# Kernel optimization log

Measured on AMD Instinct MI355X. Metric: run time of the kernel, lower is better.

## Reference

```python
import jax, jax.numpy as jnp
import numpy as np

B, N, H, E, D = 8, 2048, 1024, 8, 2048


def setup_inputs() -> dict:
    key = jax.random.key(0)
    k = jax.random.split(key, 5)
    x = jax.random.normal(k[0], (B, N, H), dtype=jnp.float32)
    Wr = jax.random.normal(k[1], (H, E), dtype=jnp.float32) * 0.02
    br = jnp.zeros((E,), dtype=jnp.float32)
    W1 = jax.random.normal(k[2], (E, H, D), dtype=jnp.float32) * 0.02
    b1 = jnp.zeros((E, D), dtype=jnp.float32)
    W2 = jax.random.normal(k[3], (E, D, H), dtype=jnp.float32) * 0.02
    b2 = jnp.zeros((E, H), dtype=jnp.float32)
    return {"x": x, "Wr": Wr, "br": br, "W1": W1, "b1": b1, "W2": W2, "b2": b2}


def reference(x, Wr, br, W1, b1, W2, b2):
    # x: [B,N,H]; router v1, top-1, eval mode (no expert dropout)
    Bx, Nx, Hx = x.shape
    Ex = Wr.shape[1]
    x_flat = x.reshape(Bx * Nx, Hx)                      # [T,H]
    logits = x_flat @ Wr + br                            # [T,E]
    probs = jax.nn.softmax(logits, axis=-1)              # [T,E]
    expert_idx = jnp.argmax(probs, axis=-1)              # [T]

    out_flat = jnp.zeros_like(x_flat)
    for e in range(Ex):  # small fixed loop over experts
        h = jax.nn.gelu(x_flat @ W1[e] + b1[e], approximate=False)  # exact erf GELU (torch default)
        eout = h @ W2[e] + b2[e]                         # [T,H]
        out_flat = jnp.where((expert_idx == e)[:, None], eout, out_flat)

    out = x + out_flat.reshape(Bx, Nx, Hx)               # residual

    p_i = probs.mean(axis=0)                             # [E]
    balance_loss = Ex * jnp.sum(p_i ** 2)
    EPS = 1e-8
    entropy = -jnp.sum(probs * jnp.log(probs + EPS), axis=-1)
    entropy_loss = entropy.mean()
    tokens_per_expert = jnp.bincount(expert_idx, length=Ex)
    return out, balance_loss, entropy_loss, tokens_per_expert
```

## Files before the change

kernel.cpp:

```cpp
#include <hip/hip_runtime.h>
#include <math.h>

#define TT 16384
#define HH 1024
#define DD 2048
#define EE 8

typedef float f32x4 __attribute__((ext_vector_type(4)));
typedef __bf16 bf16x8 __attribute__((ext_vector_type(8)));

__device__ __forceinline__ unsigned short f2bf(float f) {
  union { float f; unsigned u; } v; v.f = f;
  unsigned r = v.u + 0x7FFFu + ((v.u >> 16) & 1u);
  return (unsigned short)(r >> 16);
}

__global__ void k_init(int* counts, float* probs_sum, float* ent_sum) {
  int t = threadIdx.x;
  if (t < EE) { counts[t] = 0; probs_sum[t] = 0.f; }
  if (t == 0) *ent_sum = 0.f;
}

__global__ __launch_bounds__(256) void k_convert_x(const float* __restrict__ x,
                                                   unsigned short* __restrict__ xb) {
  size_t i = (size_t)(blockIdx.x * 256 + threadIdx.x) * 4;
  float4 v = *(const float4*)(x + i);
  ushort4 o;
  o.x = f2bf(v.x); o.y = f2bf(v.y); o.z = f2bf(v.z); o.w = f2bf(v.w);
  *(ushort4*)(xb + i) = o;
}

__global__ __launch_bounds__(256) void k_transpose(const float* __restrict__ src,
                                                   unsigned short* __restrict__ dst,
                                                   int R, int C) {
  __shared__ float tile[32][33];
  int tilesC = C / 32, tilesR = R / 32;
  int bid = blockIdx.x;
  int e = bid / (tilesR * tilesC);
  int rem = bid % (tilesR * tilesC);
  int tr = rem / tilesC, tc = rem % tilesC;
  const float* s = src + (size_t)e * R * C;
  unsigned short* d = dst + (size_t)e * R * C;
  int tx = threadIdx.x & 31, ty = threadIdx.x >> 5;
#pragma unroll
  for (int i = 0; i < 4; ++i)
    tile[ty + i * 8][tx] = s[(size_t)(tr * 32 + ty + i * 8) * C + tc * 32 + tx];
  __syncthreads();
#pragma unroll
  for (int i = 0; i < 4; ++i) {
    int rr = ty + i * 8;
    d[(size_t)(tc * 32 + rr) * R + tr * 32 + tx] = f2bf(tile[tx][rr]);
  }
}

__global__ __launch_bounds__(256) void k_router(const float* __restrict__ x,
                                                const float* __restrict__ Wr,
                                                const float* __restrict__ br,
                                                int* __restrict__ eidx,
                                                float* __restrict__ probs_sum,
                                                float* __restrict__ ent_sum,
                                                int* __restrict__ counts) {
  __shared__ float s_p[EE];
  __shared__ int   s_c[EE];
  __shared__ float s_e;
  int tid = threadIdx.x;
  if (tid < EE) { s_p[tid] = 0.f; s_c[tid] = 0; }
  if (tid == 0) s_e = 0.f;
  __syncthreads();
  int lane = tid & 63, w = tid >> 6;
  for (int tt = 0; tt < 4; ++tt) {
    int token = blockIdx.x * 16 + w * 4 + tt;
    double acc[EE];
#pragma unroll
    for (int e = 0; e < EE; ++e) acc[e] = 0.0;
    const float* xr = x + (size_t)token * HH;
    for (int i = 0; i < 16; ++i) {
      int hh = i * 64 + lane;
      double xv = (double)xr[hh];
      const float* wr = Wr + (size_t)hh * EE;
#pragma unroll
      for (int e = 0; e < EE; ++e) acc[e] += xv * (double)wr[e];
    }
#pragma unroll
    for (int off = 32; off > 0; off >>= 1) {
#pragma unroll
      for (int e = 0; e < EE; ++e) acc[e] += __shfl_down(acc[e], off);
    }
    if (lane == 0) {
      double l[EE];
#pragma unroll
      for (int e = 0; e < EE; ++e) l[e] = acc[e] + (double)br[e];
      double m = l[0]; int am = 0;
#pragma unroll
      for (int e = 1; e < EE; ++e) { if (l[e] > m) { m = l[e]; am = e; } }
      double p[EE]; double s = 0.0;
#pragma unroll
      for (int e = 0; e < EE; ++e) { p[e] = exp(l[e] - m); s += p[e]; }
      double inv = 1.0 / s; double ent = 0.0;
#pragma unroll
      for (int e = 0; e < EE; ++e) { p[e] *= inv; ent -= p[e] * log(p[e] + 1e-8); }
      eidx[token] = am;
#pragma unroll
      for (int e = 0; e < EE; ++e) atomicAdd(&s_p[e], (float)p[e]);
      atomicAdd(&s_e, (float)ent);
      atomicAdd(&s_c[am], 1);
    }
  }
  __syncthreads();
  if (tid < EE) { atomicAdd(&probs_sum[tid], s_p[tid]); atomicAdd(&counts[tid], s_c[tid]); }
  if (tid == 0) atomicAdd(ent_sum, s_e);
}

__global__ void k_scan(const int* counts, const float* probs_sum, const float* ent_sum,
                       int* offsets, int* cursor,
                       int* tileE, int* tileR0, int* tileEnd, int* nTiles,
                       float* out_scalars) {
  if (threadIdx.x != 0) return;
  int off = 0, nt = 0;
  for (int e = 0; e < EE; ++e) {
    offsets[e] = off; cursor[e] = off;
    int c = counts[e];
    for (int r = 0; r < c; r += 64) {
      tileE[nt] = e; tileR0[nt] = off + r; tileEnd[nt] = off + c; ++nt;
    }
    off += c;
  }
  offsets[EE] = off;
  *nTiles = nt;
  float bal = 0.f;
  for (int e = 0; e < EE; ++e) { float pi = probs_sum[e] / (float)TT; bal += pi * pi; }
  out_scalars[0] = (float)EE * bal;
  out_scalars[1] = *ent_sum / (float)TT;
  for (int e = 0; e < EE; ++e) out_scalars[2 + e] = (float)counts[e];
}

__global__ __launch_bounds__(256) void k_perm(const int* __restrict__ eidx,
                                              int* cursor, int* __restrict__ perm) {
  int t = blockIdx.x * 256 + threadIdx.x;
  int lane = threadIdx.x & 63;
  int mye = eidx[t];
  int pos = 0;
#pragma unroll
  for (int e = 0; e < EE; ++e) {
    unsigned long long mask = __ballot(mye == e);
    if (mask == 0ull) continue;
    int leader = __ffsll(mask) - 1;
    int base = 0;
    if (lane == leader) base = atomicAdd(&cursor[e], __popcll(mask));
    base = __shfl(base, leader);
    if (mye == e) pos = base + (int)__popcll(mask & ((1ull << lane) - 1ull));
  }
  perm[pos] = t;
}

__global__ __launch_bounds__(256) void k_gemm1(const unsigned short* __restrict__ xb,
                                               const unsigned short* __restrict__ Wt1,
                                               const float* __restrict__ b1,
                                               const int* __restrict__ perm,
                                               const int* __restrict__ tileE,
                                               const int* __restrict__ tileR0,
                                               const int* __restrict__ tileEnd,
                                               const int* __restrict__ nTiles,
                                               unsigned short* __restrict__ hbuf) {
  int tile = blockIdx.y;
  if (tile >= *nTiles) return;
  int e = tileE[tile], r0 = tileR0[tile], rend = tileEnd[tile];
  int c0 = blockIdx.x * 64;
  __shared__ __align__(16) unsigned short As[64][32];
  __shared__ __align__(16) unsigned short Bs[64][32];
  int tid = threadIdx.x, lane = tid & 63, w = tid >> 6;
  int wr = w >> 1, wc = w & 1;
  int arow = tid >> 2, aseg = tid & 3;
  int gRow = r0 + arow;
  int tok = perm[(gRow < rend) ? gRow : r0];
  const uint4* aSrc = (const uint4*)(xb + (size_t)tok * HH) + aseg;
  const uint4* bSrc = (const uint4*)(Wt1 + (size_t)e * (DD * HH) + (size_t)(c0 + arow) * HH) + aseg;
  f32x4 acc00 = {0,0,0,0}, acc01 = {0,0,0,0}, acc10 = {0,0,0,0}, acc11 = {0,0,0,0};
  int quad = lane >> 4, l16 = lane & 15;
  for (int k0 = 0; k0 < HH; k0 += 32) {
    uint4 av = aSrc[k0 >> 3];
    uint4 bv = bSrc[k0 >> 3];
    __syncthreads();
    *(uint4*)&As[arow][aseg * 8] = av;
    *(uint4*)&Bs[arow][aseg * 8] = bv;
    __syncthreads();
    bf16x8 a0 = *(const bf16x8*)&As[wr * 32 + l16][quad * 8];
    bf16x8 a1 = *(const bf16x8*)&As[wr * 32 + 16 + l16][quad * 8];
    bf16x8 b0 = *(const bf16x8*)&Bs[wc * 32 + l16][quad * 8];
    bf16x8 b1v = *(const bf16x8*)&Bs[wc * 32 + 16 + l16][quad * 8];
    acc00 = __builtin_amdgcn_mfma_f32_16x16x32_bf16(a0, b0,  acc00, 0, 0, 0);
    acc01 = __builtin_amdgcn_mfma_f32_16x16x32_bf16(a0, b1v, acc01, 0, 0, 0);
    acc10 = __builtin_amdgcn_mfma_f32_16x16x32_bf16(a1, b0,  acc10, 0, 0, 0);
    acc11 = __builtin_amdgcn_mfma_f32_16x16x32_bf16(a1, b1v, acc11, 0, 0, 0);
  }
  f32x4 accs[2][2] = {{acc00, acc01}, {acc10, acc11}};
#pragma unroll
  for (int i = 0; i < 2; ++i) {
#pragma unroll
    for (int j = 0; j < 2; ++j) {
#pragma unroll
      for (int r = 0; r < 4; ++r) {
        int row = wr * 32 + i * 16 + quad * 4 + r;
        int gr = r0 + row;
        if (gr < rend) {
          int col = c0 + wc * 32 + j * 16 + l16;
          float v = accs[i][j][r] + b1[e * DD + col];
          v = 0.5f * v * (1.0f + erff(v * 0.70710678118654752f));
          hbuf[(size_t)gr * DD + col] = f2bf(v);
        }
      }
    }
  }
}

__global__ __launch_bounds__(256) void k_gemm2(const unsigned short* __restrict__ hbuf,
                                               const unsigned short* __restrict__ Wt2,
                                               const float* __restrict__ b2,
                                               const float* __restrict__ x,
                                               const int* __restrict__ perm,
                                               const int* __restrict__ tileE,
                                               const int* __restrict__ tileR0,
                                               const int* __restrict__ tileEnd,
                                               const int* __restrict__ nTiles,
                                               float* __restrict__ outp) {
  int tile = blockIdx.y;
  if (tile >= *nTiles) return;
  int e = tileE[tile], r0 = tileR0[tile], rend = tileEnd[tile];
  int c0 = blockIdx.x * 64;
  __shared__ __align__(16) unsigned short As[64][32];
  __shared__ __align__(16) unsigned short Bs[64][32];
  int tid = threadIdx.x, lane = tid & 63, w = tid >> 6;
  int wr = w >> 1, wc = w & 1;
  int arow = tid >> 2, aseg = tid & 3;
  int gRow = r0 + arow;
  const uint4* aSrc = (const uint4*)(hbuf + (size_t)((gRow < rend) ? gRow : r0) * DD) + aseg;
  const uint4* bSrc = (const uint4*)(Wt2 + (size_t)e * (HH * DD) + (size_t)(c0 + arow) * DD) + aseg;
  f32x4 acc00 = {0,0,0,0}, acc01 = {0,0,0,0}, acc10 = {0,0,0,0}, acc11 = {0,0,0,0};
  int quad = lane >> 4, l16 = lane & 15;
  for (int k0 = 0; k0 < DD; k0 += 32) {
    uint4 av = aSrc[k0 >> 3];
    uint4 bv = bSrc[k0 >> 3];
    __syncthreads();
    *(uint4*)&As[arow][aseg * 8] = av;
    *(uint4*)&Bs[arow][aseg * 8] = bv;
    __syncthreads();
    bf16x8 a0 = *(const bf16x8*)&As[wr * 32 + l16][quad * 8];
    bf16x8 a1 = *(const bf16x8*)&As[wr * 32 + 16 + l16][quad * 8];
    bf16x8 b0 = *(const bf16x8*)&Bs[wc * 32 + l16][quad * 8];
    bf16x8 b1v = *(const bf16x8*)&Bs[wc * 32 + 16 + l16][quad * 8];
    acc00 = __builtin_amdgcn_mfma_f32_16x16x32_bf16(a0, b0,  acc00, 0, 0, 0);
    acc01 = __builtin_amdgcn_mfma_f32_16x16x32_bf16(a0, b1v, acc01, 0, 0, 0);
    acc10 = __builtin_amdgcn_mfma_f32_16x16x32_bf16(a1, b0,  acc10, 0, 0, 0);
    acc11 = __builtin_amdgcn_mfma_f32_16x16x32_bf16(a1, b1v, acc11, 0, 0, 0);
  }
  f32x4 accs[2][2] = {{acc00, acc01}, {acc10, acc11}};
#pragma unroll
  for (int i = 0; i < 2; ++i) {
#pragma unroll
    for (int j = 0; j < 2; ++j) {
#pragma unroll
      for (int r = 0; r < 4; ++r) {
        int row = wr * 32 + i * 16 + quad * 4 + r;
        int gr = r0 + row;
        if (gr < rend) {
          int tok = perm[gr];
          int col = c0 + wc * 32 + j * 16 + l16;
          size_t oi = (size_t)tok * HH + col;
          outp[oi] = x[oi] + b2[e * HH + col] + accs[i][j][r];
        }
      }
    }
  }
}

extern "C" void kernel_launch(void* const* d_in, const int* in_sizes, int n_in,
                              void* d_out, int out_size, void* d_ws, size_t ws_size,
                              hipStream_t stream) {
  const float* x  = (const float*)d_in[0];
  const float* Wr = (const float*)d_in[1];
  const float* br = (const float*)d_in[2];
  const float* W1 = (const float*)d_in[3];
  const float* b1 = (const float*)d_in[4];
  const float* W2 = (const float*)d_in[5];
  const float* b2 = (const float*)d_in[6];
  float* outp = (float*)d_out;

  char* ws = (char*)d_ws;
  int*   counts    = (int*)(ws + 0);
  int*   cursor    = (int*)(ws + 64);
  int*   nTiles    = (int*)(ws + 128);
  float* probs_sum = (float*)(ws + 192);
  float* ent_sum   = (float*)(ws + 256);
  int*   offsets   = (int*)(ws + 320);
  int*   tileE     = (int*)(ws + 512);
  int*   tileR0    = (int*)(ws + 2048);
  int*   tileEnd   = (int*)(ws + 3584);
  int*   eidx      = (int*)(ws + 8192);
  int*   perm      = (int*)(ws + 8192 + 4 * (size_t)TT);
  size_t off = 8192 + 8 * (size_t)TT;
  unsigned short* xb   = (unsigned short*)(ws + off); off += (size_t)TT * HH * 2;
  unsigned short* Wt1  = (unsigned short*)(ws + off); off += (size_t)EE * DD * HH * 2;
  unsigned short* Wt2  = (unsigned short*)(ws + off); off += (size_t)EE * HH * DD * 2;
  unsigned short* hbuf = (unsigned short*)(ws + off); off += (size_t)TT * DD * 2;

  k_init<<<1, 64, 0, stream>>>(counts, probs_sum, ent_sum);
  k_convert_x<<<(TT * HH / 4) / 256, 256, 0, stream>>>(x, xb);
  k_transpose<<<EE * (HH / 32) * (DD / 32), 256, 0, stream>>>(W1, Wt1, HH, DD);
  k_transpose<<<EE * (DD / 32) * (HH / 32), 256, 0, stream>>>(W2, Wt2, DD, HH);
  k_router<<<TT / 16, 256, 0, stream>>>(x, Wr, br, eidx, probs_sum, ent_sum, counts);
  k_scan<<<1, 64, 0, stream>>>(counts, probs_sum, ent_sum, offsets, cursor,
                               tileE, tileR0, tileEnd, nTiles, outp + (size_t)TT * HH);
  k_perm<<<TT / 256, 256, 0, stream>>>(eidx, cursor, perm);
  dim3 g1(DD / 64, 264);
  k_gemm1<<<g1, 256, 0, stream>>>(xb, Wt1, b1, perm, tileE, tileR0, tileEnd, nTiles, hbuf);
  dim3 g2(HH / 64, 264);
  k_gemm2<<<g2, 256, 0, stream>>>(hbuf, Wt2, b2, x, perm, tileE, tileR0, tileEnd, nTiles, outp);
}
```

Baseline: 717.5 us.

## Enlarge grouped GEMM tiles to 128x128 with direct global-to-LDS loads and fuse x conversion into router

Both expert GEMMs move from 64x64 to 128x128 block tiles. Each wave now computes a 4x4 grid of MFMA accumulators, so operands loaded once from LDS are reused across more outputs. Operand tiles are staged with global_load_lds, which removes the register round-trip on the way into shared memory. The separate bf16 conversion pass over x is folded into the router kernel, which already reads x, saving one full read of the activations. Larger tiles raise register pressure and waste more rows on partially filled expert tiles. The MAXTILES grid bound of 160 also assumes the tile count stays small.

After: 598.3 us. 1.2x faster.

```diff
diff --git a/kernel.cpp b/kernel.cpp
--- a/kernel.cpp
+++ b/kernel.cpp
@@ -5,6 +5,7 @@
 #define HH 1024
 #define DD 2048
 #define EE 8
+#define MAXTILES 160
 
 typedef float f32x4 __attribute__((ext_vector_type(4)));
 typedef __bf16 bf16x8 __attribute__((ext_vector_type(8)));
@@ -15,19 +16,16 @@
   return (unsigned short)(r >> 16);
 }
 
+__device__ __forceinline__ void gl2lds16(const unsigned short* g, unsigned short* l) {
+  __builtin_amdgcn_global_load_lds(
+      (const __attribute__((address_space(1))) void*)g,
+      (__attribute__((address_space(3))) void*)l, 16, 0, 0);
+}
+
 __global__ void k_init(int* counts, float* probs_sum, float* ent_sum) {
   int t = threadIdx.x;
   if (t < EE) { counts[t] = 0; probs_sum[t] = 0.f; }
   if (t == 0) *ent_sum = 0.f;
-}
-
-__global__ __launch_bounds__(256) void k_convert_x(const float* __restrict__ x,
-                                                   unsigned short* __restrict__ xb) {
-  size_t i = (size_t)(blockIdx.x * 256 + threadIdx.x) * 4;
-  float4 v = *(const float4*)(x + i);
-  ushort4 o;
-  o.x = f2bf(v.x); o.y = f2bf(v.y); o.z = f2bf(v.z); o.w = f2bf(v.w);
-  *(ushort4*)(xb + i) = o;
 }
 
 __global__ __launch_bounds__(256) void k_transpose(const float* __restrict__ src,
@@ -59,7 +57,8 @@
                                                 int* __restrict__ eidx,
                                                 float* __restrict__ probs_sum,
                                                 float* __restrict__ ent_sum,
-                                                int* __restrict__ counts) {
+                                                int* __restrict__ counts,
+                                                unsigned short* __restrict__ xb) {
   __shared__ float s_p[EE];
   __shared__ int   s_c[EE];
   __shared__ float s_e;
@@ -74,9 +73,12 @@
 #pragma unroll
     for (int e = 0; e < EE; ++e) acc[e] = 0.0;
     const float* xr = x + (size_t)token * HH;
+    unsigned short* xo = xb + (size_t)token * HH;
     for (int i = 0; i < 16; ++i) {
       int hh = i * 64 + lane;
-      double xv = (double)xr[hh];
+      float xf = xr[hh];
+      xo[hh] = f2bf(xf);
+      double xv = (double)xf;
       const float* wr = Wr + (size_t)hh * EE;
 #pragma unroll
       for (int e = 0; e < EE; ++e) acc[e] += xv * (double)wr[e];
@@ -120,7 +122,7 @@
   for (int e = 0; e < EE; ++e) {
     offsets[e] = off; cursor[e] = off;
     int c = counts[e];
-    for (int r = 0; r < c; r += 64) {
+    for (int r = 0; r < c; r += 128) {
       tileE[nt] = e; tileR0[nt] = off + r; tileEnd[nt] = off + c; ++nt;
     }
     off += c;
@@ -152,6 +154,7 @@
   }
   perm[pos] = t;
 }
+
 
 __global__ __launch_bounds__(256) void k_gemm1(const unsigned short* __restrict__ xb,
                                                const unsigned short* __restrict__ Wt1,
@@ -165,46 +168,59 @@
   int tile = blockIdx.y;
   if (tile >= *nTiles) return;
   int e = tileE[tile], r0 = tileR0[tile], rend = tileEnd[tile];
-  int c0 = blockIdx.x * 64;
-  __shared__ __align__(16) unsigned short As[64][32];
-  __shared__ __align__(16) unsigned short Bs[64][32];
+  int c0 = blockIdx.x * 128;
+  __shared__ __align__(16) unsigned short As[128 * 32];
+  __shared__ __align__(16) unsigned short Bs[128 * 32];
   int tid = threadIdx.x, lane = tid & 63, w = tid >> 6;
   int wr = w >> 1, wc = w & 1;
-  int arow = tid >> 2, aseg = tid & 3;
-  int gRow = r0 + arow;
-  int tok = perm[(gRow < rend) ? gRow : r0];
-  const uint4* aSrc = (const uint4*)(xb + (size_t)tok * HH) + aseg;
-  const uint4* bSrc = (const uint4*)(Wt1 + (size_t)e * (DD * HH) + (size_t)(c0 + arow) * HH) + aseg;
-  f32x4 acc00 = {0,0,0,0}, acc01 = {0,0,0,0}, acc10 = {0,0,0,0}, acc11 = {0,0,0,0};
   int quad = lane >> 4, l16 = lane & 15;
+  int srow = lane >> 2, seg = lane & 3;
+  int ar0 = w * 32 + srow, ar1 = ar0 + 16;
+  int g0 = r0 + ar0; if (g0 >= rend) g0 = rend - 1;
+  int g1 = r0 + ar1; if (g1 >= rend) g1 = rend - 1;
+  const unsigned short* aG0 = xb + (size_t)perm[g0] * HH + seg * 8;
+  const unsigned short* aG1 = xb + (size_t)perm[g1] * HH + seg * 8;
+  const unsigned short* bBase = Wt1 + (size_t)e * ((size_t)DD * HH);
+  const unsigned short* bG0 = bBase + (size_t)(c0 + ar0) * HH + seg * 8;
+  const unsigned short* bG1 = bBase + (size_t)(c0 + ar1) * HH + seg * 8;
+  unsigned short* aL0 = &As[(w * 32 + 0) * 32];
+  unsigned short* aL1 = &As[(w * 32 + 16) * 32];
+  unsigned short* bL0 = &Bs[(w * 32 + 0) * 32];
+  unsigned short* bL1 = &Bs[(w * 32 + 16) * 32];
+  f32x4 acc[4][4] = {};
   for (int k0 = 0; k0 < HH; k0 += 32) {
-    uint4 av = aSrc[k0 >> 3];
-    uint4 bv = bSrc[k0 >> 3];
+    gl2lds16(aG0 + k0, aL0);
+    gl2lds16(aG1 + k0, aL1);
+    gl2lds16(bG0 + k0, bL0);
+    gl2lds16(bG1 + k0, bL1);
     __syncthreads();
-    *(uint4*)&As[arow][aseg * 8] = av;
-    *(uint4*)&Bs[arow][aseg * 8] = bv;
+    bf16x8 a[4], b[4];
+#pragma unroll
+    for (int i = 0; i < 4; ++i)
+      a[i] = *(const bf16x8*)&As[(wr * 64 + i * 16 + l16) * 32 + quad * 8];
+#pragma unroll
+    for (int j = 0; j < 4; ++j)
+      b[j] = *(const bf16x8*)&Bs[(wc * 64 + j * 16 + l16) * 32 + quad * 8];
+#pragma unroll
+    for (int i = 0; i < 4; ++i)
+#pragma unroll
+      for (int j = 0; j < 4; ++j)
+        acc[i][j] = __builtin_amdgcn_mfma_f32_16x16x32_bf16(a[i], b[j], acc[i][j], 0, 0, 0);
     __syncthreads();
-    bf16x8 a0 = *(const bf16x8*)&As[wr * 32 + l16][quad * 8];
-    bf16x8 a1 = *(const bf16x8*)&As[wr * 32 + 16 + l16][quad * 8];
-    bf16x8 b0 = *(const bf16x8*)&Bs[wc * 32 + l16][quad * 8];
-    bf16x8 b1v = *(const bf16x8*)&Bs[wc * 32 + 16 + l16][quad * 8];
-    acc00 = __builtin_amdgcn_mfma_f32_16x16x32_bf16(a0, b0,  acc00, 0, 0, 0);
-    acc01 = __builtin_amdgcn_mfma_f32_16x16x32_bf16(a0, b1v, acc01, 0, 0, 0);
-    acc10 = __builtin_amdgcn_mfma_f32_16x16x32_bf16(a1, b0,  acc10, 0, 0, 0);
-    acc11 = __builtin_amdgcn_mfma_f32_16x16x32_bf16(a1, b1v, acc11, 0, 0, 0);
-  }
-  f32x4 accs[2][2] = {{acc00, acc01}, {acc10, acc11}};
-#pragma unroll
-  for (int i = 0; i < 2; ++i) {
-#pragma unroll
-    for (int j = 0; j < 2; ++j) {
-#pragma unroll
-      for (int r = 0; r < 4; ++r) {
-        int row = wr * 32 + i * 16 + quad * 4 + r;
-        int gr = r0 + row;
-        if (gr < rend) {
-          int col = c0 + wc * 32 + j * 16 + l16;
-          float v = accs[i][j][r] + b1[e * DD + col];
+  }
+  float bias[4];
+#pragma unroll
+  for (int j = 0; j < 4; ++j) bias[j] = b1[e * DD + c0 + wc * 64 + j * 16 + l16];
+#pragma unroll
+  for (int i = 0; i < 4; ++i) {
+#pragma unroll
+    for (int r = 0; r < 4; ++r) {
+      int gr = r0 + wr * 64 + i * 16 + quad * 4 + r;
+      if (gr < rend) {
+#pragma unroll
+        for (int j = 0; j < 4; ++j) {
+          int col = c0 + wc * 64 + j * 16 + l16;
+          float v = acc[i][j][r] + bias[j];
           v = 0.5f * v * (1.0f + erff(v * 0.70710678118654752f));
           hbuf[(size_t)gr * DD + col] = f2bf(v);
         }
@@ -226,47 +242,61 @@
   int tile = blockIdx.y;
   if (tile >= *nTiles) return;
   int e = tileE[tile], r0 = tileR0[tile], rend = tileEnd[tile];
-  int c0 = blockIdx.x * 64;
-  __shared__ __align__(16) unsigned short As[64][32];
-  __shared__ __align__(16) unsigned short Bs[64][32];
+  int c0 = blockIdx.x * 128;
+  __shared__ __align__(16) unsigned short As[128 * 32];
+  __shared__ __align__(16) unsigned short Bs[128 * 32];
   int tid = threadIdx.x, lane = tid & 63, w = tid >> 6;
   int wr = w >> 1, wc = w & 1;
-  int arow = tid >> 2, aseg = tid & 3;
-  int gRow = r0 + arow;
-  const uint4* aSrc = (const uint4*)(hbuf + (size_t)((gRow < rend) ? gRow : r0) * DD) + aseg;
-  const uint4* bSrc = (const uint4*)(Wt2 + (size_t)e * (HH * DD) + (size_t)(c0 + arow) * DD) + aseg;
-  f32x4 acc00 = {0,0,0,0}, acc01 = {0,0,0,0}, acc10 = {0,0,0,0}, acc11 = {0,0,0,0};
   int quad = lane >> 4, l16 = lane & 15;
+  int srow = lane >> 2, seg = lane & 3;
+  int ar0 = w * 32 + srow, ar1 = ar0 + 16;
+  int g0 = r0 + ar0; if (g0 >= rend) g0 = rend - 1;
+  int g1 = r0 + ar1; if (g1 >= rend) g1 = rend - 1;
+  const unsigned short* aG0 = hbuf + (size_t)g0 * DD + seg * 8;
+  const unsigned short* aG1 = hbuf + (size_t)g1 * DD + seg * 8;
+  const unsigned short* bBase = Wt2 + (size_t)e * ((size_t)HH * DD);
+  const unsigned short* bG0 = bBase + (size_t)(c0 + ar0) * DD + seg * 8;
+  const unsigned short* bG1 = bBase + (size_t)(c0 + ar1) * DD + seg * 8;
+  unsigned short* aL0 = &As[(w * 32 + 0) * 32];
+  unsigned short* aL1 = &As[(w * 32 + 16) * 32];
+  unsigned short* bL0 = &Bs[(w * 32 + 0) * 32];
+  unsigned short* bL1 = &Bs[(w * 32 + 16) * 32];
+  f32x4 acc[4][4] = {};
   for (int k0 = 0; k0 < DD; k0 += 32) {
-    uint4 av = aSrc[k0 >> 3];
-    uint4 bv = bSrc[k0 >> 3];
+    gl2lds16(aG0 + k0, aL0);
+    gl2lds16(aG1 + k0, aL1);
+    gl2lds16(bG0 + k0, bL0);
+    gl2lds16(bG1 + k0, bL1);
     __syncthreads();
-    *(uint4*)&As[arow][aseg * 8] = av;
-    *(uint4*)&Bs[arow][aseg * 8] = bv;
+    bf16x8 a[4], b[4];
+#pragma unroll
+    for (int i = 0; i < 4; ++i)
+      a[i] = *(const bf16x8*)&As[(wr * 64 + i * 16 + l16) * 32 + quad * 8];
+#pragma unroll
+    for (int j = 0; j < 4; ++j)
+      b[j] = *(const bf16x8*)&Bs[(wc * 64 + j * 16 + l16) * 32 + quad * 8];
+#pragma unroll
+    for (int i = 0; i < 4; ++i)
+#pragma unroll
+      for (int j = 0; j < 4; ++j)
+        acc[i][j] = __builtin_amdgcn_mfma_f32_16x16x32_bf16(a[i], b[j], acc[i][j], 0, 0, 0);
     __syncthreads();
-    bf16x8 a0 = *(const bf16x8*)&As[wr * 32 + l16][quad * 8];
-    bf16x8 a1 = *(const bf16x8*)&As[wr * 32 + 16 + l16][quad * 8];
-    bf16x8 b0 = *(const bf16x8*)&Bs[wc * 32 + l16][quad * 8];
-    bf16x8 b1v = *(const bf16x8*)&Bs[wc * 32 + 16 + l16][quad * 8];
-    acc00 = __builtin_amdgcn_mfma_f32_16x16x32_bf16(a0, b0,  acc00, 0, 0, 0);
-    acc01 = __builtin_amdgcn_mfma_f32_16x16x32_bf16(a0, b1v, acc01, 0, 0, 0);
-    acc10 = __builtin_amdgcn_mfma_f32_16x16x32_bf16(a1, b0,  acc10, 0, 0, 0);
-    acc11 = __builtin_amdgcn_mfma_f32_16x16x32_bf16(a1, b1v, acc11, 0, 0, 0);
-  }
-  f32x4 accs[2][2] = {{acc00, acc01}, {acc10, acc11}};
-#pragma unroll
-  for (int i = 0; i < 2; ++i) {
-#pragma unroll
-    for (int j = 0; j < 2; ++j) {
-#pragma unroll
-      for (int r = 0; r < 4; ++r) {
-        int row = wr * 32 + i * 16 + quad * 4 + r;
-        int gr = r0 + row;
-        if (gr < rend) {
-          int tok = perm[gr];
-          int col = c0 + wc * 32 + j * 16 + l16;
+  }
+  float bias[4];
+#pragma unroll
+  for (int j = 0; j < 4; ++j) bias[j] = b2[e * HH + c0 + wc * 64 + j * 16 + l16];
+#pragma unroll
+  for (int i = 0; i < 4; ++i) {
+#pragma unroll
+    for (int r = 0; r < 4; ++r) {
+      int gr = r0 + wr * 64 + i * 16 + quad * 4 + r;
+      if (gr < rend) {
+        int tok = perm[gr];
+#pragma unroll
+        for (int j = 0; j < 4; ++j) {
+          int col = c0 + wc * 64 + j * 16 + l16;
           size_t oi = (size_t)tok * HH + col;
-          outp[oi] = x[oi] + b2[e * HH + col] + accs[i][j][r];
+          outp[oi] = x[oi] + bias[j] + acc[i][j][r];
         }
       }
     }
@@ -304,15 +334,14 @@
   unsigned short* hbuf = (unsigned short*)(ws + off); off += (size_t)TT * DD * 2;
 
   k_init<<<1, 64, 0, stream>>>(counts, probs_sum, ent_sum);
-  k_convert_x<<<(TT * HH / 4) / 256, 256, 0, stream>>>(x, xb);
   k_transpose<<<EE * (HH / 32) * (DD / 32), 256, 0, stream>>>(W1, Wt1, HH, DD);
   k_transpose<<<EE * (DD / 32) * (HH / 32), 256, 0, stream>>>(W2, Wt2, DD, HH);
-  k_router<<<TT / 16, 256, 0, stream>>>(x, Wr, br, eidx, probs_sum, ent_sum, counts);
+  k_router<<<TT / 16, 256, 0, stream>>>(x, Wr, br, eidx, probs_sum, ent_sum, counts, xb);
   k_scan<<<1, 64, 0, stream>>>(counts, probs_sum, ent_sum, offsets, cursor,
                                tileE, tileR0, tileEnd, nTiles, outp + (size_t)TT * HH);
   k_perm<<<TT / 256, 256, 0, stream>>>(eidx, cursor, perm);
-  dim3 g1(DD / 64, 264);
+  dim3 g1(DD / 128, MAXTILES);
   k_gemm1<<<g1, 256, 0, stream>>>(xb, Wt1, b1, perm, tileE, tileR0, tileEnd, nTiles, hbuf);
-  dim3 g2(HH / 64, 264);
+  dim3 g2(HH / 128, MAXTILES);
   k_gemm2<<<g2, 256, 0, stream>>>(hbuf, Wt2, b2, x, perm, tileE, tileR0, tileEnd, nTiles, outp);
 }
```
